# Kernel tuning notes

Hardware: AMD Instinct MI355X
Metric: run time of the kernel (lower is better)

Reference implementation:

```python
import jax, jax.numpy as jnp
import numpy as np

N = 100000
E = 1600000
D = 128


def setup_inputs() -> dict:
    key = jax.random.key(0)
    ks = jax.random.split(key, 9)
    s = 1.0 / np.sqrt(D)
    return {
        "x": jax.random.normal(ks[0], (N, D), dtype=jnp.float32),
        "edge_index": jax.random.randint(ks[1], (2, E), 0, N, dtype=jnp.int64),
        # SAGEConv layer 1: lin_l (neighbor path, with bias), lin_r (root path, no bias)
        "Wl1": jax.random.normal(ks[2], (D, D), dtype=jnp.float32) * s,
        "bl1": jnp.zeros((D,), dtype=jnp.float32),
        "Wr1": jax.random.normal(ks[3], (D, D), dtype=jnp.float32) * s,
        # SAGEConv layer 2
        "Wl2": jax.random.normal(ks[4], (D, D), dtype=jnp.float32) * s,
        "bl2": jnp.zeros((D,), dtype=jnp.float32),
        "Wr2": jax.random.normal(ks[5], (D, D), dtype=jnp.float32) * s,
    }


def _sage_conv(x, src, dst, Wl, bl, Wr):
    # PyG SAGEConv, aggr='mean', root_weight=True:
    #   out = lin_l(mean_{j in N(i)} x_j) + lin_r(x_i)
    msg = x[src]                                              # [E, D] gather
    agg = jax.ops.segment_sum(msg, dst, num_segments=N)       # [N, D]
    cnt = jax.ops.segment_sum(jnp.ones((src.shape[0],), x.dtype), dst, num_segments=N)
    agg = agg / jnp.maximum(cnt, 1.0)[:, None]                # mean aggregation
    return agg @ Wl.T + bl + x @ Wr.T


def reference(x, edge_index, Wl1, bl1, Wr1, Wl2, bl2, Wr2):
    src, dst = edge_index[0], edge_index[1]
    h = jax.nn.relu(_sage_conv(x, src, dst, Wl1, bl1, Wr1))
    out = _sage_conv(h, src, dst, Wl2, bl2, Wr2)
    return out
```

## Files before the change

### kernel.cpp

```cpp
#include <hip/hip_runtime.h>
#include <stdint.h>

#define DN 128
#define NBITS 6
#define BNODES 64
#define HBMAX 2048
#define CAP 1536
#define NSL 256

__host__ __device__ static inline int divup(int a, int b){ return (a+b-1)/b; }

typedef __attribute__((ext_vector_type(8))) short bf16x8;
typedef __attribute__((ext_vector_type(4))) float floatx4;

__device__ __forceinline__ unsigned short f2bf(float f){
  unsigned int x = __float_as_uint(f);
  unsigned int r = x + 0x7fffu + ((x >> 16) & 1u);
  return (unsigned short)(r >> 16);
}
__device__ __forceinline__ unsigned int pack2(unsigned short a, unsigned short b){
  return (unsigned int)a | ((unsigned int)b << 16);
}


__global__ __launch_bounds__(256)
void convert_all(const float* __restrict__ x,
                 const float* __restrict__ w0, const float* __restrict__ w1,
                 const float* __restrict__ w2, const float* __restrict__ w3,
                 unsigned short* __restrict__ xb, unsigned short* __restrict__ Wb,
                 int* __restrict__ gcur, int nbuck, int count8){
  int i = blockIdx.x*256 + threadIdx.x;
  if (i < nbuck) gcur[i] = 0;
  const float* sp; unsigned short* dp; int off;
  if (i < count8){ sp = x; dp = xb; off = i; }
  else {
    int tid = i - count8;
    if (tid >= 8192) return;
    int mat = tid >> 11; off = tid & 2047;
    sp = (mat==0)?w0:(mat==1)?w1:(mat==2)?w2:w3;
    dp = Wb + (size_t)mat*16384;
  }
  const float4* s = (const float4*)sp + (size_t)off*2;
  float4 a = s[0], b = s[1];
  uint4 o;
  o.x = pack2(f2bf(a.x), f2bf(a.y));
  o.y = pack2(f2bf(a.z), f2bf(a.w));
  o.z = pack2(f2bf(b.x), f2bf(b.y));
  o.w = pack2(f2bf(b.z), f2bf(b.w));
  ((uint4*)dp)[off] = o;
}

__global__ __launch_bounds__(256)
void scatter_atomic(const int* __restrict__ src, const int* __restrict__ dst,
                    int* __restrict__ gcur, unsigned int* __restrict__ packed,
                    int E, int nbuck){
  __shared__ int h[HBMAX];
  __shared__ int cur[HBMAX];
  int s = blockIdx.x, t = threadIdx.x;
  for (int i=t; i<nbuck; i+=256) h[i] = 0;
  __syncthreads();
  int n4 = E >> 2, per4 = divup(n4, NSL);
  int lo = s*per4, hi = min(lo+per4, n4);
  const int4* dst4 = (const int4*)dst;
  for (int i = lo + t; i < hi; i += 256){
    int4 d4 = dst4[i];
    atomicAdd(&h[d4.x >> NBITS], 1);
    atomicAdd(&h[d4.y >> NBITS], 1);
    atomicAdd(&h[d4.z >> NBITS], 1);
    atomicAdd(&h[d4.w >> NBITS], 1);
  }
  if (s == NSL-1){
    for (int e = (n4<<2) + t; e < E; e += 256)
      atomicAdd(&h[dst[e] >> NBITS], 1);
  }
  __syncthreads();
  for (int i=t; i<nbuck; i+=256){
    int c = h[i];
    int base = c ? atomicAdd(&gcur[i], c) : 0;
    cur[i] = i*CAP + base;
  }
  __syncthreads();
  const int4* src4 = (const int4*)src;
  for (int i = lo + t; i < hi; i += 256){
    int4 d4 = dst4[i];
    int4 s4 = src4[i];
    int dd[4] = {d4.x, d4.y, d4.z, d4.w};
    int ss[4] = {s4.x, s4.y, s4.z, s4.w};
    #pragma unroll
    for (int j=0;j<4;j++){
      int d = dd[j], b = d >> NBITS;
      int pos = atomicAdd(&cur[b], 1);
      if (pos < (b+1)*CAP)
        packed[pos] = (unsigned)ss[j] | ((unsigned)(d & (BNODES-1)) << 17);
    }
  }
  if (s == NSL-1){
    for (int e = (n4<<2) + t; e < E; e += 256){
      int d = dst[e], b = d >> NBITS;
      int pos = atomicAdd(&cur[b], 1);
      if (pos < (b+1)*CAP)
        packed[pos] = (unsigned)src[e] | ((unsigned)(d & (BNODES-1)) << 17);
    }
  }
}

__global__ __launch_bounds__(256)
void node_sort(const int* __restrict__ gcur, unsigned int* __restrict__ buf,
               int2* __restrict__ nodeOff2, int n){
  __shared__ int cnts[BNODES], offs[BNODES], cursor[BNODES];
  int b = blockIdx.x, t = threadIdx.x;
  int cnt = min(gcur[b], CAP);
  int base = b*CAP;
  if (t < BNODES) cnts[t] = 0;
  __syncthreads();
  unsigned pk[6];
  #pragma unroll
  for (int k=0;k<6;k++){
    int i = t + k*256;
    if (i < cnt){
      pk[k] = buf[base + i];
      atomicAdd(&cnts[(pk[k]>>17)&63], 1);
    }
  }
  __syncthreads();
  if (t < BNODES){
    int v = cnts[t], sft = v;
    #pragma unroll
    for (int off=1; off<64; off<<=1){
      int u = __shfl_up(sft, off, 64);
      if (t >= off) sft += u;
    }
    offs[t] = sft - v; cursor[t] = sft - v;
    int node = b*BNODES + t;
    if (node < n) nodeOff2[node] = make_int2(base + sft - v, base + sft);
  }
  __syncthreads();
  #pragma unroll
  for (int k=0;k<6;k++){
    int i = t + k*256;
    if (i < cnt){
      int nd = (pk[k]>>17)&63;
      int r = atomicAdd(&cursor[nd], 1);
      buf[base + r] = pk[k] & 0x1FFFFu;
    }
  }
}

__global__ __launch_bounds__(256)
void aggregate_csr(const unsigned short* __restrict__ xb, const int2* __restrict__ nodeOff2,
                   const unsigned int* __restrict__ csr_src, unsigned short* __restrict__ aggb, int n){
  int g = (blockIdx.x*256 + threadIdx.x) >> 4;
  int l = threadIdx.x & 15;
  if (g >= n) return;
  int2 be = nodeOff2[g];
  int beg = be.x, end = be.y;
  float acc[8] = {0,0,0,0,0,0,0,0};
  #define ACCUM(u) { unsigned int w;                                   \
      w=(u).x; acc[0]+=__uint_as_float(w<<16); acc[1]+=__uint_as_float(w&0xffff0000u); \
      w=(u).y; acc[2]+=__uint_as_float(w<<16); acc[3]+=__uint_as_float(w&0xffff0000u); \
      w=(u).z; acc[4]+=__uint_as_float(w<<16); acc[5]+=__uint_as_float(w&0xffff0000u); \
      w=(u).w; acc[6]+=__uint_as_float(w<<16); acc[7]+=__uint_as_float(w&0xffff0000u); }
  int p = beg;
  for (; p+4 <= end; p += 4){
    int s0 = csr_src[p], s1 = csr_src[p+1], s2 = csr_src[p+2], s3 = csr_src[p+3];
    uint4 u0 = ((const uint4*)(xb + (size_t)s0*DN))[l];
    uint4 u1 = ((const uint4*)(xb + (size_t)s1*DN))[l];
    uint4 u2 = ((const uint4*)(xb + (size_t)s2*DN))[l];
    uint4 u3 = ((const uint4*)(xb + (size_t)s3*DN))[l];
    ACCUM(u0) ACCUM(u1) ACCUM(u2) ACCUM(u3)
  }
  for (; p < end; ++p){
    int s0 = csr_src[p];
    uint4 u0 = ((const uint4*)(xb + (size_t)s0*DN))[l];
    ACCUM(u0)
  }
  #undef ACCUM
  float inv = 1.f / fmaxf((float)(end-beg), 1.f);
  uint4 o;
  o.x = pack2(f2bf(acc[0]*inv), f2bf(acc[1]*inv));
  o.y = pack2(f2bf(acc[2]*inv), f2bf(acc[3]*inv));
  o.z = pack2(f2bf(acc[4]*inv), f2bf(acc[5]*inv));
  o.w = pack2(f2bf(acc[6]*inv), f2bf(acc[7]*inv));
  ((uint4*)(aggb + (size_t)g*DN))[l] = o;
}

template<bool RELU, bool OUT_BF16>
__global__ __launch_bounds__(256)
void gemm_mfma(const unsigned short* __restrict__ A1, const unsigned short* __restrict__ W1b,
               const unsigned short* __restrict__ A2, const unsigned short* __restrict__ W2b,
               const float* __restrict__ bias, void* __restrict__ out,
               int rt_total, int rt_per_block)
{
  int wave = threadIdx.x >> 6;
  int lane = threadIdx.x & 63;
  int m = lane & 15, quad = lane >> 4;

  bf16x8 Bf[2][2][4];
  {
    const unsigned short* Ws[2] = {W1b, W2b};
    #pragma unroll
    for (int c2=0;c2<2;c2++){
      int col = wave*32 + c2*16 + m;
      #pragma unroll
      for (int mat=0;mat<2;mat++){
        const unsigned short* wrow = Ws[mat] + (size_t)col*DN + quad*8;
        #pragma unroll
        for (int kc=0;kc<4;kc++)
          Bf[c2][mat][kc] = *(const bf16x8*)(wrow + kc*32);
      }
    }
  }
  float bv0 = bias[wave*32 + m];
  float bv1 = bias[wave*32 + 16 + m];

  int rt_begin = blockIdx.x * rt_per_block;
  int rt_end = rt_begin + rt_per_block; if (rt_end > rt_total) rt_end = rt_total;

  for (int rt = rt_begin; rt < rt_end; ++rt){
    const unsigned short* a1p = A1 + ((size_t)(rt*16 + m))*DN + quad*8;
    const unsigned short* a2p = A2 + ((size_t)(rt*16 + m))*DN + quad*8;
    bf16x8 Af[2][4];
    #pragma unroll
    for (int kc=0;kc<4;kc++){
      Af[0][kc] = *(const bf16x8*)(a1p + kc*32);
      Af[1][kc] = *(const bf16x8*)(a2p + kc*32);
    }
    __syncthreads();
    floatx4 acc0 = {0.f,0.f,0.f,0.f}, acc1 = {0.f,0.f,0.f,0.f};
    #pragma unroll
    for (int mat=0; mat<2; mat++)
      #pragma unroll
      for (int kc=0; kc<4; kc++){
        acc0 = __builtin_amdgcn_mfma_f32_16x16x32_bf16(Af[mat][kc], Bf[0][mat][kc], acc0, 0,0,0);
        acc1 = __builtin_amdgcn_mfma_f32_16x16x32_bf16(Af[mat][kc], Bf[1][mat][kc], acc1, 0,0,0);
      }
    #pragma unroll
    for (int r=0;r<4;r++){
      int row = rt*16 + quad*4 + r;
      float v0 = acc0[r] + bv0;
      float v1 = acc1[r] + bv1;
      if (RELU){ v0 = fmaxf(v0, 0.f); v1 = fmaxf(v1, 0.f); }
      if (OUT_BF16){
        unsigned short* o = (unsigned short*)out + (size_t)row*DN + wave*32 + m;
        o[0]  = f2bf(v0);
        o[16] = f2bf(v1);
      } else {
        float* o = (float*)out + (size_t)row*DN + wave*32 + m;
        o[0]  = v0;
        o[16] = v1;
      }
    }
  }
}


extern "C" void kernel_launch(void* const* d_in, const int* in_sizes, int n_in,
                              void* d_out, int out_size, void* d_ws, size_t ws_size,
                              hipStream_t stream) {
  const float* x   = (const float*)d_in[0];
  const int*   ei  = (const int*)d_in[1];
  const float* Wl1 = (const float*)d_in[2];
  const float* bl1 = (const float*)d_in[3];
  const float* Wr1 = (const float*)d_in[4];
  const float* Wl2 = (const float*)d_in[5];
  const float* bl2 = (const float*)d_in[6];
  const float* Wr2 = (const float*)d_in[7];

  const int n = in_sizes[0] / DN;
  const int E = in_sizes[1] / 2;
  const int* src = ei;
  const int* dst = ei + E;
  const int nbuck = divup(n, BNODES);

  char* ws = (char*)d_ws;
  char* ws_end = ws + ws_size;
  int* gcur = (int*)ws;  ws += (size_t)HBMAX*4;
  ws = (char*)(((uintptr_t)ws + 255) & ~(uintptr_t)255);
  unsigned int* packed = (unsigned int*)ws; ws += (size_t)nbuck*CAP*4;
  ws = (char*)(((uintptr_t)ws + 255) & ~(uintptr_t)255);
  int2* nodeOff2   = (int2*)ws; ws += (size_t)n*8;
  ws = (char*)(((uintptr_t)ws + 255) & ~(uintptr_t)255);
  unsigned short* Wb   = (unsigned short*)ws; ws += 4*16384*2;
  unsigned short* xb   = (unsigned short*)ws; ws += (size_t)n*DN*2;
  unsigned short* aggb = (unsigned short*)ws; ws += (size_t)n*DN*2;
  unsigned short* hb = xb;
  if (ws + (size_t)n*DN*2 <= ws_end) { hb = (unsigned short*)ws; ws += (size_t)n*DN*2; }

  unsigned short* Wl1b = Wb;
  unsigned short* Wr1b = Wb + 16384;
  unsigned short* Wl2b = Wb + 2*16384;
  unsigned short* Wr2b = Wb + 3*16384;

  const int count8 = n*DN/8;
  convert_all<<<divup(count8 + 8192, 256),256,0,stream>>>(x, Wl1, Wr1, Wl2, Wr2, xb, Wb, gcur, nbuck, count8);
  scatter_atomic<<<NSL,  256,0,stream>>>(src, dst, gcur, packed, E, nbuck);
  node_sort     <<<nbuck,256,0,stream>>>(gcur, packed, nodeOff2, n);

  const int rt_total = n / 16;
  const int rt_per_block = 5;
  const int gblocks = divup(rt_total, rt_per_block);
  const int agrid = divup(n*16, 256);

  aggregate_csr<<<agrid,256,0,stream>>>(xb, nodeOff2, packed, aggb, n);
  gemm_mfma<true, true ><<<gblocks,256,0,stream>>>(aggb, Wl1b, xb, Wr1b, bl1, hb, rt_total, rt_per_block);
  aggregate_csr<<<agrid,256,0,stream>>>(hb, nodeOff2, packed, aggb, n);
  gemm_mfma<false,false><<<gblocks,256,0,stream>>>(aggb, Wl2b, hb, Wr2b, bl2, d_out, rt_total, rt_per_block);
}
```

Baseline: 336.0 us.

## Replace bucketed CSR build with per-node fixed slots; stage GEMM output in LDS

Replaces the two-pass bucket scatter plus per-bucket node sort with one kernel that uses global atomics on per-node counters to write source ids into fixed 64-slot rows per destination node. Aggregation then reads degree and slots directly, loading indices as int4. This drops a kernel launch and the in-LDS sort, but it silently truncates any node with more than 64 in-edges. With an average in-degree of 16 that overflow is unlikely but possible. Separately, the GEMM epilogue now stages results in shared memory and writes coalesced 16-byte stores, at the cost of extra barriers.

```diff
diff --git a/kernel.cpp b/kernel.cpp
--- a/kernel.cpp
+++ b/kernel.cpp
@@ -2,11 +2,7 @@
 #include <stdint.h>
 
 #define DN 128
-#define NBITS 6
-#define BNODES 64
-#define HBMAX 2048
-#define CAP 1536
-#define NSL 256
+#define CAPN 64
 
 __host__ __device__ static inline int divup(int a, int b){ return (a+b-1)/b; }
 
@@ -28,9 +24,9 @@
                  const float* __restrict__ w0, const float* __restrict__ w1,
                  const float* __restrict__ w2, const float* __restrict__ w3,
                  unsigned short* __restrict__ xb, unsigned short* __restrict__ Wb,
-                 int* __restrict__ gcur, int nbuck, int count8){
+                 int* __restrict__ cnt, int n, int count8){
   int i = blockIdx.x*256 + threadIdx.x;
-  if (i < nbuck) gcur[i] = 0;
+  if (i < n) cnt[i] = 0;
   const float* sp; unsigned short* dp; int off;
   if (i < count8){ sp = x; dp = xb; off = i; }
   else {
@@ -51,131 +47,60 @@
 }
 
 __global__ __launch_bounds__(256)
-void scatter_atomic(const int* __restrict__ src, const int* __restrict__ dst,
-                    int* __restrict__ gcur, unsigned int* __restrict__ packed,
-                    int E, int nbuck){
-  __shared__ int h[HBMAX];
-  __shared__ int cur[HBMAX];
-  int s = blockIdx.x, t = threadIdx.x;
-  for (int i=t; i<nbuck; i+=256) h[i] = 0;
-  __syncthreads();
-  int n4 = E >> 2, per4 = divup(n4, NSL);
-  int lo = s*per4, hi = min(lo+per4, n4);
-  const int4* dst4 = (const int4*)dst;
-  for (int i = lo + t; i < hi; i += 256){
-    int4 d4 = dst4[i];
-    atomicAdd(&h[d4.x >> NBITS], 1);
-    atomicAdd(&h[d4.y >> NBITS], 1);
-    atomicAdd(&h[d4.z >> NBITS], 1);
-    atomicAdd(&h[d4.w >> NBITS], 1);
-  }
-  if (s == NSL-1){
-    for (int e = (n4<<2) + t; e < E; e += 256)
-      atomicAdd(&h[dst[e] >> NBITS], 1);
-  }
-  __syncthreads();
-  for (int i=t; i<nbuck; i+=256){
-    int c = h[i];
-    int base = c ? atomicAdd(&gcur[i], c) : 0;
-    cur[i] = i*CAP + base;
-  }
-  __syncthreads();
-  const int4* src4 = (const int4*)src;
-  for (int i = lo + t; i < hi; i += 256){
-    int4 d4 = dst4[i];
-    int4 s4 = src4[i];
+void scatter_node(const int* __restrict__ src, const int* __restrict__ dst,
+                  int* __restrict__ cnt, int* __restrict__ slots, int E){
+  int i = blockIdx.x*256 + threadIdx.x;
+  int n4 = E >> 2;
+  if (i < n4){
+    int4 d4 = ((const int4*)dst)[i];
+    int4 s4 = ((const int4*)src)[i];
     int dd[4] = {d4.x, d4.y, d4.z, d4.w};
     int ss[4] = {s4.x, s4.y, s4.z, s4.w};
     #pragma unroll
     for (int j=0;j<4;j++){
-      int d = dd[j], b = d >> NBITS;
-      int pos = atomicAdd(&cur[b], 1);
-      if (pos < (b+1)*CAP)
-        packed[pos] = (unsigned)ss[j] | ((unsigned)(d & (BNODES-1)) << 17);
-    }
-  }
-  if (s == NSL-1){
-    for (int e = (n4<<2) + t; e < E; e += 256){
-      int d = dst[e], b = d >> NBITS;
-      int pos = atomicAdd(&cur[b], 1);
-      if (pos < (b+1)*CAP)
-        packed[pos] = (unsigned)src[e] | ((unsigned)(d & (BNODES-1)) << 17);
-    }
-  }
-}
-
-__global__ __launch_bounds__(256)
-void node_sort(const int* __restrict__ gcur, unsigned int* __restrict__ buf,
-               int2* __restrict__ nodeOff2, int n){
-  __shared__ int cnts[BNODES], offs[BNODES], cursor[BNODES];
-  int b = blockIdx.x, t = threadIdx.x;
-  int cnt = min(gcur[b], CAP);
-  int base = b*CAP;
-  if (t < BNODES) cnts[t] = 0;
-  __syncthreads();
-  unsigned pk[6];
-  #pragma unroll
-  for (int k=0;k<6;k++){
-    int i = t + k*256;
-    if (i < cnt){
-      pk[k] = buf[base + i];
-      atomicAdd(&cnts[(pk[k]>>17)&63], 1);
-    }
-  }
-  __syncthreads();
-  if (t < BNODES){
-    int v = cnts[t], sft = v;
-    #pragma unroll
-    for (int off=1; off<64; off<<=1){
-      int u = __shfl_up(sft, off, 64);
-      if (t >= off) sft += u;
-    }
-    offs[t] = sft - v; cursor[t] = sft - v;
-    int node = b*BNODES + t;
-    if (node < n) nodeOff2[node] = make_int2(base + sft - v, base + sft);
-  }
-  __syncthreads();
-  #pragma unroll
-  for (int k=0;k<6;k++){
-    int i = t + k*256;
-    if (i < cnt){
-      int nd = (pk[k]>>17)&63;
-      int r = atomicAdd(&cursor[nd], 1);
-      buf[base + r] = pk[k] & 0x1FFFFu;
-    }
-  }
-}
-
-__global__ __launch_bounds__(256)
-void aggregate_csr(const unsigned short* __restrict__ xb, const int2* __restrict__ nodeOff2,
-                   const unsigned int* __restrict__ csr_src, unsigned short* __restrict__ aggb, int n){
+      int pos = atomicAdd(&cnt[dd[j]], 1);
+      if (pos < CAPN)
+        slots[(size_t)dd[j]*CAPN + pos] = ss[j];
+    }
+  }
+  int e = (n4<<2) + i;
+  if (i < (E & 3)){
+    int d = dst[e];
+    int pos = atomicAdd(&cnt[d], 1);
+    if (pos < CAPN) slots[(size_t)d*CAPN + pos] = src[e];
+  }
+}
+
+__global__ __launch_bounds__(256)
+void aggregate_csr(const unsigned short* __restrict__ xb, const int* __restrict__ cnt,
+                   const int* __restrict__ slots, unsigned short* __restrict__ aggb, int n){
   int g = (blockIdx.x*256 + threadIdx.x) >> 4;
   int l = threadIdx.x & 15;
   if (g >= n) return;
-  int2 be = nodeOff2[g];
-  int beg = be.x, end = be.y;
+  int deg = min(cnt[g], CAPN);
+  const int* sl = slots + (size_t)g*CAPN;
   float acc[8] = {0,0,0,0,0,0,0,0};
   #define ACCUM(u) { unsigned int w;                                   \
       w=(u).x; acc[0]+=__uint_as_float(w<<16); acc[1]+=__uint_as_float(w&0xffff0000u); \
       w=(u).y; acc[2]+=__uint_as_float(w<<16); acc[3]+=__uint_as_float(w&0xffff0000u); \
       w=(u).z; acc[4]+=__uint_as_float(w<<16); acc[5]+=__uint_as_float(w&0xffff0000u); \
       w=(u).w; acc[6]+=__uint_as_float(w<<16); acc[7]+=__uint_as_float(w&0xffff0000u); }
-  int p = beg;
-  for (; p+4 <= end; p += 4){
-    int s0 = csr_src[p], s1 = csr_src[p+1], s2 = csr_src[p+2], s3 = csr_src[p+3];
-    uint4 u0 = ((const uint4*)(xb + (size_t)s0*DN))[l];
-    uint4 u1 = ((const uint4*)(xb + (size_t)s1*DN))[l];
-    uint4 u2 = ((const uint4*)(xb + (size_t)s2*DN))[l];
-    uint4 u3 = ((const uint4*)(xb + (size_t)s3*DN))[l];
+  int p = 0;
+  for (; p+4 <= deg; p += 4){
+    int4 si = *(const int4*)(sl + p);
+    uint4 u0 = ((const uint4*)(xb + (size_t)si.x*DN))[l];
+    uint4 u1 = ((const uint4*)(xb + (size_t)si.y*DN))[l];
+    uint4 u2 = ((const uint4*)(xb + (size_t)si.z*DN))[l];
+    uint4 u3 = ((const uint4*)(xb + (size_t)si.w*DN))[l];
     ACCUM(u0) ACCUM(u1) ACCUM(u2) ACCUM(u3)
   }
-  for (; p < end; ++p){
-    int s0 = csr_src[p];
+  for (; p < deg; ++p){
+    int s0 = sl[p];
     uint4 u0 = ((const uint4*)(xb + (size_t)s0*DN))[l];
     ACCUM(u0)
   }
   #undef ACCUM
-  float inv = 1.f / fmaxf((float)(end-beg), 1.f);
+  float inv = 1.f / fmaxf((float)deg, 1.f);
   uint4 o;
   o.x = pack2(f2bf(acc[0]*inv), f2bf(acc[1]*inv));
   o.y = pack2(f2bf(acc[2]*inv), f2bf(acc[3]*inv));
@@ -191,8 +116,10 @@
                const float* __restrict__ bias, void* __restrict__ out,
                int rt_total, int rt_per_block)
 {
-  int wave = threadIdx.x >> 6;
-  int lane = threadIdx.x & 63;
+  __shared__ unsigned char obuf[8192];
+  int t = threadIdx.x;
+  int wave = t >> 6;
+  int lane = t & 63;
   int m = lane & 15, quad = lane >> 4;
 
   bf16x8 Bf[2][2][4];
@@ -234,21 +161,34 @@
         acc0 = __builtin_amdgcn_mfma_f32_16x16x32_bf16(Af[mat][kc], Bf[0][mat][kc], acc0, 0,0,0);
         acc1 = __builtin_amdgcn_mfma_f32_16x16x32_bf16(Af[mat][kc], Bf[1][mat][kc], acc1, 0,0,0);
       }
-    #pragma unroll
-    for (int r=0;r<4;r++){
-      int row = rt*16 + quad*4 + r;
-      float v0 = acc0[r] + bv0;
-      float v1 = acc1[r] + bv1;
-      if (RELU){ v0 = fmaxf(v0, 0.f); v1 = fmaxf(v1, 0.f); }
-      if (OUT_BF16){
-        unsigned short* o = (unsigned short*)out + (size_t)row*DN + wave*32 + m;
-        o[0]  = f2bf(v0);
-        o[16] = f2bf(v1);
-      } else {
-        float* o = (float*)out + (size_t)row*DN + wave*32 + m;
-        o[0]  = v0;
-        o[16] = v1;
-      }
+    if (OUT_BF16){
+      unsigned short (*ob)[128] = (unsigned short (*)[128])obuf;
+      #pragma unroll
+      for (int r=0;r<4;r++){
+        float v0 = acc0[r] + bv0;
+        float v1 = acc1[r] + bv1;
+        if (RELU){ v0 = fmaxf(v0, 0.f); v1 = fmaxf(v1, 0.f); }
+        ob[quad*4+r][wave*32 + m]      = f2bf(v0);
+        ob[quad*4+r][wave*32 + 16 + m] = f2bf(v1);
+      }
+      __syncthreads();
+      ((uint4*)((unsigned short*)out + (size_t)rt*16*DN))[t & 255] = ((const uint4*)obuf)[t & 255];
+      __syncthreads();
+    } else {
+      float (*of)[128] = (float (*)[128])obuf;
+      #pragma unroll
+      for (int r=0;r<4;r++){
+        float v0 = acc0[r] + bv0;
+        float v1 = acc1[r] + bv1;
+        if (RELU){ v0 = fmaxf(v0, 0.f); v1 = fmaxf(v1, 0.f); }
+        of[quad*4+r][wave*32 + m]      = v0;
+        of[quad*4+r][wave*32 + 16 + m] = v1;
+      }
+      __syncthreads();
+      uint4* og = (uint4*)((float*)out + (size_t)rt*16*DN);
+      og[t]       = ((const uint4*)obuf)[t];
+      og[t + 256] = ((const uint4*)obuf)[t + 256];
+      __syncthreads();
     }
   }
 }
@@ -270,15 +210,12 @@
   const int E = in_sizes[1] / 2;
   const int* src = ei;
   const int* dst = ei + E;
-  const int nbuck = divup(n, BNODES);
 
   char* ws = (char*)d_ws;
   char* ws_end = ws + ws_size;
-  int* gcur = (int*)ws;  ws += (size_t)HBMAX*4;
+  int* cnt = (int*)ws;  ws += (size_t)n*4;
   ws = (char*)(((uintptr_t)ws + 255) & ~(uintptr_t)255);
-  unsigned int* packed = (unsigned int*)ws; ws += (size_t)nbuck*CAP*4;
-  ws = (char*)(((uintptr_t)ws + 255) & ~(uintptr_t)255);
-  int2* nodeOff2   = (int2*)ws; ws += (size_t)n*8;
+  int* slots = (int*)ws; ws += (size_t)n*CAPN*4;
   ws = (char*)(((uintptr_t)ws + 255) & ~(uintptr_t)255);
   unsigned short* Wb   = (unsigned short*)ws; ws += 4*16384*2;
   unsigned short* xb   = (unsigned short*)ws; ws += (size_t)n*DN*2;
@@ -292,17 +229,16 @@
   unsigned short* Wr2b = Wb + 3*16384;
 
   const int count8 = n*DN/8;
-  convert_all<<<divup(count8 + 8192, 256),256,0,stream>>>(x, Wl1, Wr1, Wl2, Wr2, xb, Wb, gcur, nbuck, count8);
-  scatter_atomic<<<NSL,  256,0,stream>>>(src, dst, gcur, packed, E, nbuck);
-  node_sort     <<<nbuck,256,0,stream>>>(gcur, packed, nodeOff2, n);
+  convert_all<<<divup(count8 + 8192, 256),256,0,stream>>>(x, Wl1, Wr1, Wl2, Wr2, xb, Wb, cnt, n, count8);
+  scatter_node<<<divup(E/4, 256),256,0,stream>>>(src, dst, cnt, slots, E);
 
   const int rt_total = n / 16;
   const int rt_per_block = 5;
   const int gblocks = divup(rt_total, rt_per_block);
   const int agrid = divup(n*16, 256);
 
-  aggregate_csr<<<agrid,256,0,stream>>>(xb, nodeOff2, packed, aggb, n);
+  aggregate_csr<<<agrid,256,0,stream>>>(xb, cnt, slots, aggb, n);
   gemm_mfma<true, true ><<<gblocks,256,0,stream>>>(aggb, Wl1b, xb, Wr1b, bl1, hb, rt_total, rt_per_block);
-  aggregate_csr<<<agrid,256,0,stream>>>(hb, nodeOff2, packed, aggb, n);
+  aggregate_csr<<<agrid,256,0,stream>>>(hb, cnt, slots, aggb, n);
   gemm_mfma<false,false><<<gblocks,256,0,stream>>>(aggb, Wl2b, hb, Wr2b, bl2, d_out, rt_total, rt_per_block);
 }
```

Result: slower. 430.4 us (+28.1%).
